# Optimization experiments

Measured on AMD Instinct MI355X. Metric: run time of the kernel, lower is better.

## Reference

```python
import jax, jax.numpy as jnp
import numpy as np

B, T, H, W, C = 8, 32, 64, 64, 3
F = 24        # conv filters
U = 128       # lstm units
O = 1         # output units

def _conv(x, w, b):
    # x: [N,H,W,Cin], w: [3,3,Cin,Cout], SAME padding, linear activation
    y = jax.lax.conv_general_dilated(x, w, window_strides=(1, 1), padding='SAME',
                                     dimension_numbers=('NHWC', 'HWIO', 'NHWC'))
    return y + b

def setup_inputs() -> dict:
    key = jax.random.key(0)
    ks = jax.random.split(key, 16)
    s = lambda *shape: 0.05
    inp = {
        'x': jax.random.normal(ks[0], (B, T, H, W, C), dtype=jnp.float32),
        'conv1_w': jax.random.normal(ks[1], (3, 3, C, F), dtype=jnp.float32) * 0.1,
        'conv1_b': jnp.zeros((F,), jnp.float32),
        'conv2_w': jax.random.normal(ks[2], (3, 3, F, F), dtype=jnp.float32) * 0.1,
        'conv2_b': jnp.zeros((F,), jnp.float32),
        'Wf': jax.random.normal(ks[3], (F + U, U), dtype=jnp.float32) * 0.08,
        'bf': jnp.zeros((U,), jnp.float32),
        'Wi': jax.random.normal(ks[4], (F + U, U), dtype=jnp.float32) * 0.08,
        'bi': jnp.zeros((U,), jnp.float32),
        'Wc': jax.random.normal(ks[5], (F + U, U), dtype=jnp.float32) * 0.08,
        'bc': jnp.zeros((U,), jnp.float32),
        'Wo': jax.random.normal(ks[6], (F + U, U), dtype=jnp.float32) * 0.08,
        'bo': jnp.zeros((U,), jnp.float32),
        'out_w': jax.random.normal(ks[7], (U, O), dtype=jnp.float32) * 0.08,
        'out_b': jnp.zeros((O,), jnp.float32),
    }
    return inp

def reference(x, conv1_w, conv1_b, conv2_w, conv2_b, Wf, bf, Wi, bi, Wc, bc, Wo, bo, out_w, out_b):
    b, t, h, w, c = x.shape
    # CNN block (per-frame): two linear 3x3 convs, no pooling inside block
    xr = x.reshape(b * t, h, w, c)
    xr = _conv(xr, conv1_w, conv1_b)
    xr = _conv(xr, conv2_w, conv2_b)
    # TimeDistributed(GlobalAvgPool2D): mean over H,W -> [B,T,F]
    feat = xr.reshape(b, t, h, w, -1).mean(axis=(2, 3))

    # custom LSTM recurrence over time via scan
    def step(carry, xt):
        hs, cs = carry
        z = jnp.concatenate([xt, hs], axis=-1)           # [B, F+U]
        f = jax.nn.sigmoid(z @ Wf + bf)
        i = jax.nn.sigmoid(z @ Wi + bi)
        g = jnp.tanh(z @ Wc + bc)
        o = jax.nn.sigmoid(z @ Wo + bo)
        c_new = cs * f + i * g
        h_new = jnp.tanh(c_new) * o
        return (h_new, c_new), h_new

    h0 = jnp.zeros((b, Wf.shape[1]), x.dtype)
    c0 = jnp.zeros((b, Wf.shape[1]), x.dtype)
    _, hs = jax.lax.scan(step, (h0, c0), jnp.swapaxes(feat, 0, 1))  # [T,B,U]
    hs = jnp.swapaxes(hs, 0, 1)                                     # [B,T,U]
    return hs @ out_w + out_b                                       # [B,T,O]
```

## Files before the change

kernel.cpp:

```cpp
#include <hip/hip_runtime.h>
#include <math.h>

#define Bb 8
#define Tt 32
#define Hh 64
#define Ww 64
#define Cc 3
#define Ff 24
#define Uu 128

__global__ void convfeat_kernel(const float* __restrict__ x,
                                const float* __restrict__ w1, const float* __restrict__ b1,
                                const float* __restrict__ w2, const float* __restrict__ b2,
                                const float* __restrict__ Wf, const float* __restrict__ bf,
                                const float* __restrict__ Wi, const float* __restrict__ bi,
                                const float* __restrict__ Wc, const float* __restrict__ bc,
                                const float* __restrict__ Wo, const float* __restrict__ bo,
                                float* __restrict__ G) {
    int n = blockIdx.x;
    const float* xf = x + (size_t)n * (Hh * Ww * Cc);
    int tid  = threadIdx.x;
    int row  = tid >> 2;
    int part = tid & 3;

    __shared__ float partial[256][3];
    __shared__ float rowsum[64][3];
    __shared__ float colv[64][12];
    __shared__ float st[75];
    __shared__ float yst[24][9];
    __shared__ float feats[24];

    float s0 = 0.f, s1 = 0.f, s2 = 0.f;
    const float4* p4 = (const float4*)(xf + (row * Ww + part * 16) * Cc);
#pragma unroll
    for (int i = 0; i < 12; ++i) {
        float4 v = p4[i];
        int j = i * 4;
        float vv[4] = {v.x, v.y, v.z, v.w};
#pragma unroll
        for (int l = 0; l < 4; ++l) {
            int c = (j + l) % 3;
            if (c == 0) s0 += vv[l]; else if (c == 1) s1 += vv[l]; else s2 += vv[l];
        }
    }
    partial[tid][0] = s0; partial[tid][1] = s1; partial[tid][2] = s2;

    if (tid < 64) {
        int r = tid;
#pragma unroll
        for (int w4 = 0; w4 < 4; ++w4) {
            int w = (w4 < 2) ? w4 : 60 + w4;
#pragma unroll
            for (int c = 0; c < 3; ++c) colv[r][w4 * 3 + c] = xf[(r * Ww + w) * Cc + c];
        }
    }
    __syncthreads();

    if (part == 0) {
#pragma unroll
        for (int c = 0; c < 3; ++c)
            rowsum[row][c] = partial[tid][c] + partial[tid + 1][c]
                           + partial[tid + 2][c] + partial[tid + 3][c];
    }
    __syncthreads();

    if (tid < 3) {
        float t = 0.f;
        for (int r = 0; r < 64; ++r) t += rowsum[r][tid];
        st[tid * 25 + 0] = t;
    }
    if (tid >= 4 && tid < 16) {
        int k = tid - 4; int ri = k / 3, c = k % 3;
        int r = (ri < 2) ? ri : 60 + ri;
        st[c * 25 + 1 + ri] = rowsum[r][c];
    }
    if (tid >= 64 && tid < 76) {
        int k = tid - 64;
        float t = 0.f;
        for (int r = 0; r < 64; ++r) t += colv[r][k];
        int wi = k / 3, c = k % 3;
        st[c * 25 + 5 + wi] = t;
    }
    if (tid >= 128 && tid < 176) {
        int k = tid - 128; int pos = k / 3, c = k % 3;
        int ri = pos >> 2, wi = pos & 3;
        int r = (ri < 2) ? ri : 60 + ri;
        int w = (wi < 2) ? wi : 60 + wi;
        st[c * 25 + 9 + pos] = xf[(r * Ww + w) * Cc + c];
    }
    __syncthreads();

    if (tid < 24) {
        int f = tid;
        float Sy = 0, r0 = 0, r63 = 0, c0 = 0, c63 = 0, y00 = 0, y0W = 0, yH0 = 0, yHW = 0;
        for (int c = 0; c < 3; ++c) {
            const float* S = st + c * 25;
            float Sx = S[0];
            float rX[4] = {S[1], S[2], S[3], S[4]};
            float cX[4] = {S[5], S[6], S[7], S[8]};
            const float* X = S + 9;
            #define W1(p, q) w1[(((p) * 3 + (q)) * 3 + c) * 24 + f]
#pragma unroll
            for (int p = 0; p < 3; ++p)
#pragma unroll
                for (int q = 0; q < 3; ++q) {
                    float t = Sx;
                    if (p == 0) t -= rX[3];
                    if (p == 2) t -= rX[0];
                    if (q == 0) t -= cX[3];
                    if (q == 2) t -= cX[0];
                    if (p == 0 && q == 0) t += X[3 * 4 + 3];
                    if (p == 0 && q == 2) t += X[3 * 4 + 0];
                    if (p == 2 && q == 0) t += X[0 * 4 + 3];
                    if (p == 2 && q == 2) t += X[0 * 4 + 0];
                    Sy += W1(p, q) * t;
                }
#pragma unroll
            for (int q = 0; q < 3; ++q) {
                float Rr0  = rX[0] - ((q == 0) ? X[0 * 4 + 3] : 0.f) - ((q == 2) ? X[0 * 4 + 0] : 0.f);
                float Rr1  = rX[1] - ((q == 0) ? X[1 * 4 + 3] : 0.f) - ((q == 2) ? X[1 * 4 + 0] : 0.f);
                float Rr62 = rX[2] - ((q == 0) ? X[2 * 4 + 3] : 0.f) - ((q == 2) ? X[2 * 4 + 0] : 0.f);
                float Rr63 = rX[3] - ((q == 0) ? X[3 * 4 + 3] : 0.f) - ((q == 2) ? X[3 * 4 + 0] : 0.f);
                r0  += W1(1, q) * Rr0  + W1(2, q) * Rr1;
                r63 += W1(0, q) * Rr62 + W1(1, q) * Rr63;
            }
#pragma unroll
            for (int p = 0; p < 3; ++p) {
                float Rc0  = cX[0] - ((p == 0) ? X[3 * 4 + 0] : 0.f) - ((p == 2) ? X[0 * 4 + 0] : 0.f);
                float Rc1  = cX[1] - ((p == 0) ? X[3 * 4 + 1] : 0.f) - ((p == 2) ? X[0 * 4 + 1] : 0.f);
                float Rc62 = cX[2] - ((p == 0) ? X[3 * 4 + 2] : 0.f) - ((p == 2) ? X[0 * 4 + 2] : 0.f);
                float Rc63 = cX[3] - ((p == 0) ? X[3 * 4 + 3] : 0.f) - ((p == 2) ? X[0 * 4 + 3] : 0.f);
                c0  += W1(p, 1) * Rc0  + W1(p, 2) * Rc1;
                c63 += W1(p, 0) * Rc62 + W1(p, 1) * Rc63;
            }
            y00 += W1(1, 1) * X[0 * 4 + 0] + W1(1, 2) * X[0 * 4 + 1]
                 + W1(2, 1) * X[1 * 4 + 0] + W1(2, 2) * X[1 * 4 + 1];
            y0W += W1(1, 0) * X[0 * 4 + 2] + W1(1, 1) * X[0 * 4 + 3]
                 + W1(2, 0) * X[1 * 4 + 2] + W1(2, 1) * X[1 * 4 + 3];
            yH0 += W1(0, 1) * X[2 * 4 + 0] + W1(0, 2) * X[2 * 4 + 1]
                 + W1(1, 1) * X[3 * 4 + 0] + W1(1, 2) * X[3 * 4 + 1];
            yHW += W1(0, 0) * X[2 * 4 + 2] + W1(0, 1) * X[2 * 4 + 3]
                 + W1(1, 0) * X[3 * 4 + 2] + W1(1, 1) * X[3 * 4 + 3];
            #undef W1
        }
        float bb = b1[f];
        yst[f][0] = Sy + 4096.f * bb;
        yst[f][1] = r0 + 64.f * bb;
        yst[f][2] = r63 + 64.f * bb;
        yst[f][3] = c0 + 64.f * bb;
        yst[f][4] = c63 + 64.f * bb;
        yst[f][5] = y00 + bb; yst[f][6] = y0W + bb;
        yst[f][7] = yH0 + bb; yst[f][8] = yHW + bb;
    }
    __syncthreads();

    if (tid < 24) {
        int g = tid;
        float acc = 0.f;
        for (int f = 0; f < 24; ++f) {
            float Sy = yst[f][0], rY0 = yst[f][1], rY63 = yst[f][2], cY0 = yst[f][3], cY63 = yst[f][4];
            float yc00 = yst[f][5], yc0W = yst[f][6], ycH0 = yst[f][7], ycHW = yst[f][8];
#pragma unroll
            for (int p = 0; p < 3; ++p)
#pragma unroll
                for (int q = 0; q < 3; ++q) {
                    float t = Sy;
                    if (p == 0) t -= rY63;
                    if (p == 2) t -= rY0;
                    if (q == 0) t -= cY63;
                    if (q == 2) t -= cY0;
                    if (p == 0 && q == 0) t += ycHW;
                    if (p == 0 && q == 2) t += ycH0;
                    if (p == 2 && q == 0) t += yc0W;
                    if (p == 2 && q == 2) t += yc00;
                    acc += w2[(((p * 3 + q) * 24 + f) * 24) + g] * t;
                }
        }
        feats[g] = b2[g] + acc * (1.f / 4096.f);
    }
    __syncthreads();

    int b = n >> 5, t = n & 31;
    float* Gdst = G + ((size_t)(t * Bb + b)) * 512;
#pragma unroll
    for (int rep = 0; rep < 2; ++rep) {
        int col = tid + rep * 256;
        int gg = col >> 7, u = col & 127;
        const float* W    = (gg == 0) ? Wf : (gg == 1) ? Wi : (gg == 2) ? Wc : Wo;
        const float* bias = (gg == 0) ? bf : (gg == 1) ? bi : (gg == 2) ? bc : bo;
        float acc = bias[u];
#pragma unroll
        for (int k = 0; k < Ff; ++k) acc += feats[k] * W[k * Uu + u];
        Gdst[u * 4 + gg] = acc;
    }
}

#define LD8(d0,d1,d2,d3,d4,d5,d6,d7) \
  "global_load_dword v" #d0 ", v[46:47], off\n\t" \
  "global_load_dword v" #d1 ", v[46:47], off offset:512\n\t" \
  "global_load_dword v" #d2 ", v[46:47], off offset:1024\n\t" \
  "global_load_dword v" #d3 ", v[46:47], off offset:1536\n\t" \
  "global_load_dword v" #d4 ", v[46:47], off offset:2048\n\t" \
  "global_load_dword v" #d5 ", v[46:47], off offset:2560\n\t" \
  "global_load_dword v" #d6 ", v[46:47], off offset:3072\n\t" \
  "global_load_dword v" #d7 ", v[46:47], off offset:3584\n\t"
#define BUMP \
  "v_add_co_u32 v46, vcc, 0x1000, v46\n\t" \
  "v_addc_co_u32 v47, vcc, 0, v47, vcc\n\t"
#define PA2(rA,fA,iA,cA,oA, rB,fB,iB,cB,oB) \
  "v_readlane_b32 s20, v32, " #rA "\n\t" \
  "v_readlane_b32 s21, v32, " #rB "\n\t" \
  "v_fmac_f32 v34, s20, v" #fA "\n\t" \
  "v_fmac_f32 v35, s20, v" #iA "\n\t" \
  "v_fmac_f32 v36, s20, v" #cA "\n\t" \
  "v_fmac_f32 v37, s20, v" #oA "\n\t" \
  "v_fmac_f32 v34, s21, v" #fB "\n\t" \
  "v_fmac_f32 v35, s21, v" #iB "\n\t" \
  "v_fmac_f32 v36, s21, v" #cB "\n\t" \
  "v_fmac_f32 v37, s21, v" #oB "\n\t"

__global__ __launch_bounds__(512) void lstm_kernel(
        const float* __restrict__ G,
        const float* __restrict__ Wf, const float* __restrict__ Wi,
        const float* __restrict__ Wc, const float* __restrict__ Wo,
        const float* __restrict__ out_w, const float* __restrict__ out_b,
        float* __restrict__ out) {
    int b   = blockIdx.x;
    int tid = threadIdx.x;
    int w   = tid >> 6;
    int l   = tid & 63;
    int q   = w >> 1;
    int uc  = ((w & 1) << 6) | l;
    int u   = (q << 5) | (l & 31);

    __shared__ __align__(16) float Gl[Tt][Uu * 4];
    __shared__ __align__(16) float prt[2][4][Uu][4];
    __shared__ __align__(16) float hist[Tt][Uu];

    {
        int r  = tid >> 4;
        int cc = (tid & 15) * 32;
        const float4* src = (const float4*)(G + ((size_t)(r * Bb + b)) * 512 + cc);
        float4* dst = (float4*)(&Gl[r][cc]);
#pragma unroll
        for (int i = 0; i < 8; ++i) dst[i] = src[i];
    }
    __syncthreads();

    const float* Wfp = Wf + (size_t)(Ff + 32 * q) * Uu + uc;
    const float* Wip = Wi + (size_t)(Ff + 32 * q) * Uu + uc;
    const float* Wcp = Wc + (size_t)(Ff + 32 * q) * Uu + uc;
    const float* Wop = Wo + (size_t)(Ff + 32 * q) * Uu + uc;
    unsigned f_lo = (unsigned)(uintptr_t)Wfp, f_hi = (unsigned)((uintptr_t)Wfp >> 32);
    unsigned i_lo = (unsigned)(uintptr_t)Wip, i_hi = (unsigned)((uintptr_t)Wip >> 32);
    unsigned c_lo = (unsigned)(uintptr_t)Wcp, c_hi = (unsigned)((uintptr_t)Wcp >> 32);
    unsigned o_lo = (unsigned)(uintptr_t)Wop, o_hi = (unsigned)((uintptr_t)Wop >> 32);
    unsigned pw = (unsigned)(uintptr_t)&prt[0][q][uc][0];
    unsigned pr = (unsigned)(uintptr_t)&prt[0][0][u][0];
    unsigned ga = (unsigned)(uintptr_t)&Gl[0][u * 4];
    unsigned ha = (unsigned)(uintptr_t)&hist[0][u];

    asm volatile(
        "v_mov_b32 v46, %0\n\t" "v_mov_b32 v47, %1\n\t"
        LD8(64,65,66,67,68,69,70,71) BUMP
        LD8(72,73,74,75,76,77,78,79) BUMP
        LD8(80,81,82,83,84,85,86,87) BUMP
        LD8(88,89,90,91,92,93,94,95)
        "v_mov_b32 v46, %2\n\t" "v_mov_b32 v47, %3\n\t"
        LD8(96,97,98,99,100,101,102,103) BUMP
        LD8(104,105,106,107,108,109,110,111) BUMP
        LD8(112,113,114,115,116,117,118,119) BUMP
        LD8(120,121,122,123,124,125,126,127)
        "v_mov_b32 v46, %4\n\t" "v_mov_b32 v47, %5\n\t"
        LD8(128,129,130,131,132,133,134,135) BUMP
        LD8(136,137,138,139,140,141,142,143) BUMP
        LD8(144,145,146,147,148,149,150,151) BUMP
        LD8(152,153,154,155,156,157,158,159)
        "v_mov_b32 v46, %6\n\t" "v_mov_b32 v47, %7\n\t"
        LD8(160,161,162,163,164,165,166,167) BUMP
        LD8(168,169,170,171,172,173,174,175) BUMP
        LD8(176,177,178,179,180,181,182,183) BUMP
        LD8(184,185,186,187,188,189,190,191)
        "s_waitcnt vmcnt(0)\n\t"
        "v_mov_b32 v40, %8\n\t"
        "v_mov_b32 v41, %9\n\t"
        "v_mov_b32 v42, %10\n\t"
        "v_mov_b32 v43, %11\n\t"
        "v_mov_b32 v32, 0\n\t"
        "v_mov_b32 v33, 0\n\t"
        "s_mov_b32 s22, 32\n\t"
        "Lstep_%=:\n\t"
        "v_mov_b32 v34, 0\n\t" "v_mov_b32 v35, 0\n\t"
        "v_mov_b32 v36, 0\n\t" "v_mov_b32 v37, 0\n\t"
        PA2(0,64,96,128,160,   1,65,97,129,161)
        PA2(2,66,98,130,162,   3,67,99,131,163)
        PA2(4,68,100,132,164,  5,69,101,133,165)
        PA2(6,70,102,134,166,  7,71,103,135,167)
        PA2(8,72,104,136,168,  9,73,105,137,169)
        PA2(10,74,106,138,170, 11,75,107,139,171)
        PA2(12,76,108,140,172, 13,77,109,141,173)
        PA2(14,78,110,142,174, 15,79,111,143,175)
        PA2(16,80,112,144,176, 17,81,113,145,177)
        PA2(18,82,114,146,178, 19,83,115,147,179)
        PA2(20,84,116,148,180, 21,85,117,149,181)
        PA2(22,86,118,150,182, 23,87,119,151,183)
        PA2(24,88,120,152,184, 25,89,121,153,185)
        PA2(26,90,122,154,186, 27,91,123,155,187)
        PA2(28,92,124,156,188, 29,93,125,157,189)
        PA2(30,94,126,158,190, 31,95,127,159,191)
        "ds_write_b128 v40, v[34:37]\n\t"
        "s_waitcnt lgkmcnt(0)\n\t"
        "s_barrier\n\t"
        "ds_read_b128 v[44:47], v41\n\t"
        "ds_read_b128 v[48:51], v41 offset:2048\n\t"
        "ds_read_b128 v[52:55], v41 offset:4096\n\t"
        "ds_read_b128 v[56:59], v41 offset:6144\n\t"
        "ds_read_b128 v[60:63], v42\n\t"
        "s_waitcnt lgkmcnt(0)\n\t"
        "v_add_f32 v44, v44, v48\n\t" "v_add_f32 v45, v45, v49\n\t"
        "v_add_f32 v46, v46, v50\n\t" "v_add_f32 v47, v47, v51\n\t"
        "v_add_f32 v52, v52, v56\n\t" "v_add_f32 v53, v53, v57\n\t"
        "v_add_f32 v54, v54, v58\n\t" "v_add_f32 v55, v55, v59\n\t"
        "v_add_f32 v44, v44, v52\n\t" "v_add_f32 v45, v45, v53\n\t"
        "v_add_f32 v46, v46, v54\n\t" "v_add_f32 v47, v47, v55\n\t"
        "v_add_f32 v44, v44, v60\n\t" "v_add_f32 v45, v45, v61\n\t"
        "v_add_f32 v46, v46, v62\n\t" "v_add_f32 v47, v47, v63\n\t"
        "v_mul_f32 v48, 0xbfb8aa3b, v44\n\t"
        "v_mul_f32 v49, 0xbfb8aa3b, v45\n\t"
        "v_mul_f32 v50, 0xc038aa3b, v46\n\t"
        "v_mul_f32 v51, 0xbfb8aa3b, v47\n\t"
        "v_exp_f32 v48, v48\n\t" "v_exp_f32 v49, v49\n\t"
        "v_exp_f32 v50, v50\n\t" "v_exp_f32 v51, v51\n\t"
        "s_nop 1\n\t"
        "v_add_f32 v48, 1.0, v48\n\t" "v_add_f32 v49, 1.0, v49\n\t"
        "v_add_f32 v50, 1.0, v50\n\t" "v_add_f32 v51, 1.0, v51\n\t"
        "v_rcp_f32 v48, v48\n\t" "v_rcp_f32 v49, v49\n\t"
        "v_rcp_f32 v50, v50\n\t" "v_rcp_f32 v51, v51\n\t"
        "s_nop 1\n\t"
        "v_mul_f32 v50, 2.0, v50\n\t"
        "v_add_f32 v50, -1.0, v50\n\t"
        "v_mul_f32 v33, v33, v48\n\t"
        "v_fmac_f32 v33, v49, v50\n\t"
        "v_mul_f32 v52, 0xc038aa3b, v33\n\t"
        "v_exp_f32 v52, v52\n\t"
        "s_nop 1\n\t"
        "v_add_f32 v52, 1.0, v52\n\t"
        "v_rcp_f32 v52, v52\n\t"
        "s_nop 1\n\t"
        "v_mul_f32 v52, 2.0, v52\n\t"
        "v_add_f32 v52, -1.0, v52\n\t"
        "v_mul_f32 v32, v52, v51\n\t"
        "ds_write_b32 v43, v32\n\t"
        "v_add_u32 v42, 0x800, v42\n\t"
        "v_add_u32 v43, 0x200, v43\n\t"
        "v_xor_b32 v40, 0x2000, v40\n\t"
        "v_xor_b32 v41, 0x2000, v41\n\t"
        "s_sub_u32 s22, s22, 1\n\t"
        "s_cmp_lg_u32 s22, 0\n\t"
        "s_cbranch_scc1 Lstep_%=\n\t"
        "s_waitcnt lgkmcnt(0)\n\t"
        :
        : "v"(f_lo), "v"(f_hi), "v"(i_lo), "v"(i_hi),
          "v"(c_lo), "v"(c_hi), "v"(o_lo), "v"(o_hi),
          "v"(pw), "v"(pr), "v"(ga), "v"(ha)
        : "memory", "vcc", "scc", "s20", "s21", "s22",
          "v32","v33","v34","v35","v36","v37","v38","v39",
          "v40","v41","v42","v43","v44","v45","v46","v47",
          "v48","v49","v50","v51","v52","v53","v54","v55",
          "v56","v57","v58","v59","v60","v61","v62","v63",
          "v64","v65","v66","v67","v68","v69","v70","v71",
          "v72","v73","v74","v75","v76","v77","v78","v79",
          "v80","v81","v82","v83","v84","v85","v86","v87",
          "v88","v89","v90","v91","v92","v93","v94","v95",
          "v96","v97","v98","v99","v100","v101","v102","v103",
          "v104","v105","v106","v107","v108","v109","v110","v111",
          "v112","v113","v114","v115","v116","v117","v118","v119",
          "v120","v121","v122","v123","v124","v125","v126","v127",
          "v128","v129","v130","v131","v132","v133","v134","v135",
          "v136","v137","v138","v139","v140","v141","v142","v143",
          "v144","v145","v146","v147","v148","v149","v150","v151",
          "v152","v153","v154","v155","v156","v157","v158","v159",
          "v160","v161","v162","v163","v164","v165","v166","v167",
          "v168","v169","v170","v171","v172","v173","v174","v175",
          "v176","v177","v178","v179","v180","v181","v182","v183",
          "v184","v185","v186","v187","v188","v189","v190","v191");

    __syncthreads();

    int tt = tid >> 4, j = tid & 15;
    const float4* hh = (const float4*)(&hist[tt][j * 8]);
    float4 a0q = hh[0], a1q = hh[1];
    const float* owp = out_w + j * 8;
    float pwv = a0q.x * owp[0] + a0q.y * owp[1] + a0q.z * owp[2] + a0q.w * owp[3]
              + a1q.x * owp[4] + a1q.y * owp[5] + a1q.z * owp[6] + a1q.w * owp[7];
#pragma unroll
    for (int off = 8; off > 0; off >>= 1) pwv += __shfl_down(pwv, off, 16);
    if (j == 0) out[b * Tt + tt] = pwv + out_b[0];
}

extern "C" void kernel_launch(void* const* d_in, const int* in_sizes, int n_in,
                              void* d_out, int out_size, void* d_ws, size_t ws_size,
                              hipStream_t stream) {
    const float* x   = (const float*)d_in[0];
    const float* w1  = (const float*)d_in[1];
    const float* b1  = (const float*)d_in[2];
    const float* w2  = (const float*)d_in[3];
    const float* b2  = (const float*)d_in[4];
    const float* Wf  = (const float*)d_in[5];
    const float* bf  = (const float*)d_in[6];
    const float* Wi  = (const float*)d_in[7];
    const float* bi  = (const float*)d_in[8];
    const float* Wc  = (const float*)d_in[9];
    const float* bc  = (const float*)d_in[10];
    const float* Wo  = (const float*)d_in[11];
    const float* bo  = (const float*)d_in[12];
    const float* ow  = (const float*)d_in[13];
    const float* ob  = (const float*)d_in[14];
    float* out = (float*)d_out;

    float* G = (float*)d_ws;

    convfeat_kernel<<<Bb * Tt, 256, 0, stream>>>(x, w1, b1, w2, b2,
                                                 Wf, bf, Wi, bi, Wc, bc, Wo, bo, G);
    lstm_kernel<<<Bb, 512, 0, stream>>>(G, Wf, Wi, Wc, Wo, ow, ob, out);
}
```

Measured before the change: 47.00 us.

## Replace readlane-broadcast recurrent matvec with LDS h-broadcast and packed FMA

Instead of broadcasting each h element from a lane with v_readlane into SGPRs and issuing scalar-operand FMACs, each step now writes h into a double-buffered LDS vector and every lane reads its 32-element slice with ds_read_b128. The dot products use v_pk_fma_f32 with split even/odd accumulators that are summed at the end, halving the FMA instruction count and removing readlane serialization. This adds LDS reads per step and an extra ds_write of h, and it reorders the float accumulation.

```diff
diff --git a/kernel.cpp b/kernel.cpp
--- a/kernel.cpp
+++ b/kernel.cpp
@@ -207,17 +207,11 @@
 #define BUMP \
   "v_add_co_u32 v46, vcc, 0x1000, v46\n\t" \
   "v_addc_co_u32 v47, vcc, 0, v47, vcc\n\t"
-#define PA2(rA,fA,iA,cA,oA, rB,fB,iB,cB,oB) \
-  "v_readlane_b32 s20, v32, " #rA "\n\t" \
-  "v_readlane_b32 s21, v32, " #rB "\n\t" \
-  "v_fmac_f32 v34, s20, v" #fA "\n\t" \
-  "v_fmac_f32 v35, s20, v" #iA "\n\t" \
-  "v_fmac_f32 v36, s20, v" #cA "\n\t" \
-  "v_fmac_f32 v37, s20, v" #oA "\n\t" \
-  "v_fmac_f32 v34, s21, v" #fB "\n\t" \
-  "v_fmac_f32 v35, s21, v" #iB "\n\t" \
-  "v_fmac_f32 v36, s21, v" #cB "\n\t" \
-  "v_fmac_f32 v37, s21, v" #oB "\n\t"
+#define PKQ(f0,f1,i0,i1,c0,c1,o0,o1,h0,h1) \
+  "v_pk_fma_f32 v[34:35], v[" #f0 ":" #f1 "], v[" #h0 ":" #h1 "], v[34:35]\n\t" \
+  "v_pk_fma_f32 v[36:37], v[" #i0 ":" #i1 "], v[" #h0 ":" #h1 "], v[36:37]\n\t" \
+  "v_pk_fma_f32 v[38:39], v[" #c0 ":" #c1 "], v[" #h0 ":" #h1 "], v[38:39]\n\t" \
+  "v_pk_fma_f32 v[40:41], v[" #o0 ":" #o1 "], v[" #h0 ":" #h1 "], v[40:41]\n\t"
 
 __global__ __launch_bounds__(512) void lstm_kernel(
         const float* __restrict__ G,
@@ -233,9 +227,10 @@
     int uc  = ((w & 1) << 6) | l;
     int u   = (q << 5) | (l & 31);
 
-    __shared__ __align__(16) float Gl[Tt][Uu * 4];
-    __shared__ __align__(16) float prt[2][4][Uu][4];
-    __shared__ __align__(16) float hist[Tt][Uu];
+    __shared__ __align__(16)    float Gl[Tt][Uu * 4];
+    __shared__ __align__(16384) float prt[2][4][Uu][4];
+    __shared__ __align__(16)    float hist[Tt][Uu];
+    __shared__ __align__(1024)  float hsb[2][Uu];
 
     {
         int r  = tid >> 4;
@@ -245,6 +240,7 @@
 #pragma unroll
         for (int i = 0; i < 8; ++i) dst[i] = src[i];
     }
+    if (tid < Uu) hsb[0][tid] = 0.f;
     __syncthreads();
 
     const float* Wfp = Wf + (size_t)(Ff + 32 * q) * Uu + uc;
@@ -255,10 +251,12 @@
     unsigned i_lo = (unsigned)(uintptr_t)Wip, i_hi = (unsigned)((uintptr_t)Wip >> 32);
     unsigned c_lo = (unsigned)(uintptr_t)Wcp, c_hi = (unsigned)((uintptr_t)Wcp >> 32);
     unsigned o_lo = (unsigned)(uintptr_t)Wop, o_hi = (unsigned)((uintptr_t)Wop >> 32);
-    unsigned pw = (unsigned)(uintptr_t)&prt[0][q][uc][0];
-    unsigned pr = (unsigned)(uintptr_t)&prt[0][0][u][0];
-    unsigned ga = (unsigned)(uintptr_t)&Gl[0][u * 4];
-    unsigned ha = (unsigned)(uintptr_t)&hist[0][u];
+    unsigned pw  = (unsigned)(uintptr_t)&prt[0][q][uc][0];
+    unsigned pr  = (unsigned)(uintptr_t)&prt[0][0][u][0];
+    unsigned ga  = (unsigned)(uintptr_t)&Gl[0][u * 4];
+    unsigned ha  = (unsigned)(uintptr_t)&hist[0][u];
+    unsigned hra = (unsigned)(uintptr_t)&hsb[0][q * 32];
+    unsigned hwa = (unsigned)(uintptr_t)&hsb[1][u];
 
     asm volatile(
         "v_mov_b32 v46, %0\n\t" "v_mov_b32 v47, %1\n\t"
@@ -282,40 +280,57 @@
         LD8(176,177,178,179,180,181,182,183) BUMP
         LD8(184,185,186,187,188,189,190,191)
         "s_waitcnt vmcnt(0)\n\t"
-        "v_mov_b32 v40, %8\n\t"
-        "v_mov_b32 v41, %9\n\t"
-        "v_mov_b32 v42, %10\n\t"
-        "v_mov_b32 v43, %11\n\t"
-        "v_mov_b32 v32, 0\n\t"
+        "v_mov_b32 v24, %8\n\t"
+        "v_mov_b32 v25, %9\n\t"
+        "v_mov_b32 v26, %10\n\t"
+        "v_mov_b32 v27, %11\n\t"
+        "v_mov_b32 v28, %12\n\t"
+        "v_mov_b32 v29, %13\n\t"
         "v_mov_b32 v33, 0\n\t"
         "s_mov_b32 s22, 32\n\t"
         "Lstep_%=:\n\t"
+        "ds_read_b128 v[44:47], v28\n\t"
+        "ds_read_b128 v[48:51], v28 offset:16\n\t"
+        "ds_read_b128 v[52:55], v28 offset:32\n\t"
+        "ds_read_b128 v[56:59], v28 offset:48\n\t"
         "v_mov_b32 v34, 0\n\t" "v_mov_b32 v35, 0\n\t"
         "v_mov_b32 v36, 0\n\t" "v_mov_b32 v37, 0\n\t"
-        PA2(0,64,96,128,160,   1,65,97,129,161)
-        PA2(2,66,98,130,162,   3,67,99,131,163)
-        PA2(4,68,100,132,164,  5,69,101,133,165)
-        PA2(6,70,102,134,166,  7,71,103,135,167)
-        PA2(8,72,104,136,168,  9,73,105,137,169)
-        PA2(10,74,106,138,170, 11,75,107,139,171)
-        PA2(12,76,108,140,172, 13,77,109,141,173)
-        PA2(14,78,110,142,174, 15,79,111,143,175)
-        PA2(16,80,112,144,176, 17,81,113,145,177)
-        PA2(18,82,114,146,178, 19,83,115,147,179)
-        PA2(20,84,116,148,180, 21,85,117,149,181)
-        PA2(22,86,118,150,182, 23,87,119,151,183)
-        PA2(24,88,120,152,184, 25,89,121,153,185)
-        PA2(26,90,122,154,186, 27,91,123,155,187)
-        PA2(28,92,124,156,188, 29,93,125,157,189)
-        PA2(30,94,126,158,190, 31,95,127,159,191)
-        "ds_write_b128 v40, v[34:37]\n\t"
+        "v_mov_b32 v38, 0\n\t" "v_mov_b32 v39, 0\n\t"
+        "v_mov_b32 v40, 0\n\t" "v_mov_b32 v41, 0\n\t"
+        "s_waitcnt lgkmcnt(0)\n\t"
+        PKQ(64,65, 96,97, 128,129, 160,161, 44,45)
+        PKQ(66,67, 98,99, 130,131, 162,163, 46,47)
+        PKQ(68,69, 100,101, 132,133, 164,165, 48,49)
+        PKQ(70,71, 102,103, 134,135, 166,167, 50,51)
+        PKQ(72,73, 104,105, 136,137, 168,169, 52,53)
+        PKQ(74,75, 106,107, 138,139, 170,171, 54,55)
+        PKQ(76,77, 108,109, 140,141, 172,173, 56,57)
+        PKQ(78,79, 110,111, 142,143, 174,175, 58,59)
+        "ds_read_b128 v[44:47], v28 offset:64\n\t"
+        "ds_read_b128 v[48:51], v28 offset:80\n\t"
+        "ds_read_b128 v[52:55], v28 offset:96\n\t"
+        "ds_read_b128 v[56:59], v28 offset:112\n\t"
+        "ds_read_b128 v[60:63], v26\n\t"
+        "s_waitcnt lgkmcnt(1)\n\t"
+        PKQ(80,81, 112,113, 144,145, 176,177, 44,45)
+        PKQ(82,83, 114,115, 146,147, 178,179, 46,47)
+        PKQ(84,85, 116,117, 148,149, 180,181, 48,49)
+        PKQ(86,87, 118,119, 150,151, 182,183, 50,51)
+        PKQ(88,89, 120,121, 152,153, 184,185, 52,53)
+        PKQ(90,91, 122,123, 154,155, 186,187, 54,55)
+        PKQ(92,93, 124,125, 156,157, 188,189, 56,57)
+        PKQ(94,95, 126,127, 158,159, 190,191, 58,59)
+        "v_add_f32 v34, v34, v35\n\t"
+        "v_add_f32 v35, v36, v37\n\t"
+        "v_add_f32 v36, v38, v39\n\t"
+        "v_add_f32 v37, v40, v41\n\t"
+        "ds_write_b128 v24, v[34:37]\n\t"
         "s_waitcnt lgkmcnt(0)\n\t"
         "s_barrier\n\t"
-        "ds_read_b128 v[44:47], v41\n\t"
-        "ds_read_b128 v[48:51], v41 offset:2048\n\t"
-        "ds_read_b128 v[52:55], v41 offset:4096\n\t"
-        "ds_read_b128 v[56:59], v41 offset:6144\n\t"
-        "ds_read_b128 v[60:63], v42\n\t"
+        "ds_read_b128 v[44:47], v25\n\t"
+        "ds_read_b128 v[48:51], v25 offset:2048\n\t"
+        "ds_read_b128 v[52:55], v25 offset:4096\n\t"
+        "ds_read_b128 v[56:59], v25 offset:6144\n\t"
         "s_waitcnt lgkmcnt(0)\n\t"
         "v_add_f32 v44, v44, v48\n\t" "v_add_f32 v45, v45, v49\n\t"
         "v_add_f32 v46, v46, v50\n\t" "v_add_f32 v47, v47, v51\n\t"
@@ -350,11 +365,14 @@
         "v_mul_f32 v52, 2.0, v52\n\t"
         "v_add_f32 v52, -1.0, v52\n\t"
         "v_mul_f32 v32, v52, v51\n\t"
-        "ds_write_b32 v43, v32\n\t"
-        "v_add_u32 v42, 0x800, v42\n\t"
-        "v_add_u32 v43, 0x200, v43\n\t"
-        "v_xor_b32 v40, 0x2000, v40\n\t"
-        "v_xor_b32 v41, 0x2000, v41\n\t"
+        "ds_write_b32 v29, v32\n\t"
+        "ds_write_b32 v27, v32\n\t"
+        "v_add_u32 v26, 0x800, v26\n\t"
+        "v_add_u32 v27, 0x200, v27\n\t"
+        "v_xor_b32 v24, 0x2000, v24\n\t"
+        "v_xor_b32 v25, 0x2000, v25\n\t"
+        "v_xor_b32 v28, 0x200, v28\n\t"
+        "v_xor_b32 v29, 0x200, v29\n\t"
         "s_sub_u32 s22, s22, 1\n\t"
         "s_cmp_lg_u32 s22, 0\n\t"
         "s_cbranch_scc1 Lstep_%=\n\t"
@@ -362,8 +380,9 @@
         :
         : "v"(f_lo), "v"(f_hi), "v"(i_lo), "v"(i_hi),
           "v"(c_lo), "v"(c_hi), "v"(o_lo), "v"(o_hi),
-          "v"(pw), "v"(pr), "v"(ga), "v"(ha)
-        : "memory", "vcc", "scc", "s20", "s21", "s22",
+          "v"(pw), "v"(pr), "v"(ga), "v"(ha), "v"(hra), "v"(hwa)
+        : "memory", "vcc", "scc", "s22",
+          "v24","v25","v26","v27","v28","v29","v30","v31",
           "v32","v33","v34","v35","v36","v37","v38","v39",
           "v40","v41","v42","v43","v44","v45","v46","v47",
           "v48","v49","v50","v51","v52","v53","v54","v55",
```

New measurement: 40.40 us. -14.0%, faster.
